# Kernel optimization log

Hardware: AMD Instinct MI355X
Metric: run time of the kernel (lower is better)

The kernel has to match this reference:

```python
import jax, jax.numpy as jnp
import numpy as np

NUM_HEADS = 8
SCALE = 1.0  # args.pos_mlp_scale


def setup_inputs() -> dict:
    key = jax.random.key(0)
    ks = jax.random.split(key, 6)
    B, N, dim = 2, 384, 256
    hid = dim // 2

    def xavier(k, fan_in, fan_out):
        lim = np.sqrt(6.0 / (fan_in + fan_out)).astype(np.float32)
        return jax.random.uniform(k, (fan_in, fan_out), jnp.float32, -lim, lim)

    return {
        "x": jax.random.normal(ks[0], (B, N, dim), jnp.float32),
        "pos": jax.random.normal(ks[1], (B, N, 3), jnp.float32),
        "mask": jnp.zeros((B, N), dtype=bool),  # True = padded position
        "qkv_w": xavier(ks[2], dim, 3 * dim),
        "qkv_b": jnp.zeros((3 * dim,), jnp.float32),
        "pm_w1": xavier(ks[3], 1, hid),
        "pm_b1": jnp.zeros((hid,), jnp.float32),
        "pm_w2": xavier(ks[4], hid, dim),
        "pm_b2": jnp.zeros((dim,), jnp.float32),
        "out_w": xavier(ks[5], dim, dim),
        "out_b": jnp.zeros((dim,), jnp.float32),
    }


def reference(x, pos, mask, qkv_w, qkv_b, pm_w1, pm_b1, pm_w2, pm_b2, out_w, out_b):
    B, N, dim = x.shape
    H = NUM_HEADS
    hd = dim // H

    qkv = x @ qkv_w + qkv_b                                  # [B,N,3*dim]
    x_q, x_k, x_v = jnp.split(qkv, 3, axis=-1)

    rel = pos[:, :, None, :] - pos[:, None, :, :]            # [B,N,N,3]
    # use_distance=True: safe L2 norm (zero subgradient on the diagonal)
    sq = jnp.sum(rel * rel, axis=-1, keepdims=True)          # [B,N,N,1]
    d = jnp.sqrt(jnp.where(sq > 0, sq, 1.0)) * (sq > 0)
    rel_pos = SCALE * (jax.nn.relu(d @ pm_w1 + pm_b1) @ pm_w2 + pm_b2)  # [B,N,N,dim]

    # attn_weight_type == 'normal': w[b,i,j] = k_i * q_j + rel_pos[b,i,j]
    w = x_k[:, :, None, :] * x_q[:, None, :, :] + rel_pos    # [B,N,N,dim]
    w = w.reshape(B, N, N, H, hd)

    pair_mask = (mask[:, :, None] & mask[:, None, :])[:, :, :, None, None]
    w = jnp.where(pair_mask, -jnp.inf, w)
    w = jax.nn.softmax(w, axis=2)                            # softmax over j

    # value_without_relpos=False: v[b,i,j] = x_v[b,j] + rel_pos[b,i,j]
    v = (x_v[:, None, :, :] + rel_pos).reshape(B, N, N, H, hd)
    out = jnp.sum(v * w, axis=2).reshape(B, N, dim)          # reduce over j
    return out @ out_w + out_b
```

## Files before the change

### kernel.cpp

```cpp
#include <hip/hip_runtime.h>
#include <hip/hip_bf16.h>

#define BB 2
#define NN 384
#define DIM 256
#define HID 128
#define ROWS (BB*NN)
#define LOG2E 1.4426950408889634f

typedef __attribute__((ext_vector_type(8))) short bf16x8;
typedef __attribute__((ext_vector_type(4))) float f32x4;

static __device__ __forceinline__ unsigned int f2bf(float f) {
    unsigned int u = __builtin_bit_cast(unsigned int, f);
    return (u + 0x7FFFu + ((u >> 16) & 1u)) >> 16;
}

__global__ __launch_bounds__(256) void qkv_gemm(const float* __restrict__ x,
        const float* __restrict__ w, const float* __restrict__ bias,
        float* __restrict__ q, float* __restrict__ k, float* __restrict__ v,
        const float* __restrict__ w2, unsigned short* __restrict__ w2t) {
    __shared__ float xs[6][DIM];
    const int r0 = blockIdx.x * 6;
    const int t = threadIdx.x;

    {
        int g = blockIdx.x * 256 + t;
        w2t[(g & 255) * HID + (g >> 8)] = (unsigned short)f2bf(w2[g]);
    }

    #pragma unroll
    for (int i = 0; i < 6; ++i) xs[i][t] = x[(r0 + i) * DIM + t];
    __syncthreads();
    float acc[6][3];
    #pragma unroll
    for (int r = 0; r < 6; ++r) { acc[r][0]=0.f; acc[r][1]=0.f; acc[r][2]=0.f; }
    for (int kk0 = 0; kk0 < DIM; kk0 += 4) {
        float4 xv[6];
        #pragma unroll
        for (int r = 0; r < 6; ++r) xv[r] = *(const float4*)&xs[r][kk0];
        #pragma unroll
        for (int kk = 0; kk < 4; ++kk) {
            float w0  = w[(kk0+kk)*768 + t];
            float w1v = w[(kk0+kk)*768 + t + 256];
            float w2v = w[(kk0+kk)*768 + t + 512];
            #pragma unroll
            for (int r = 0; r < 6; ++r) {
                float xr = kk==0?xv[r].x : kk==1?xv[r].y : kk==2?xv[r].z : xv[r].w;
                acc[r][0] += xr*w0; acc[r][1] += xr*w1v; acc[r][2] += xr*w2v;
            }
        }
    }
    const float bq = bias[t], bk = bias[t+256], bv = bias[t+512];
    #pragma unroll
    for (int r = 0; r < 6; ++r) {
        q[(r0+r)*DIM + t] = acc[r][0] + bq;
        k[(r0+r)*DIM + t] = acc[r][1] + bk;
        v[(r0+r)*DIM + t] = acc[r][2] + bv;
    }
}

__global__ __launch_bounds__(512, 4) void attn_main(
        const float* __restrict__ q,
        const float* __restrict__ k,
        const float* __restrict__ v,
        const float* __restrict__ pos,
        const unsigned char* __restrict__ mask,
        const float* __restrict__ w1,
        const float* __restrict__ b1,
        const unsigned short* __restrict__ w2t,
        const float* __restrict__ b2,
        float* __restrict__ out_pre)
{
    __shared__ char smem[65536];
    unsigned short (*w2l)[HID] = (unsigned short (*)[HID])smem;
    unsigned short (*hl)[HID]  = (unsigned short (*)[HID])smem;
    float* dl  = (float*)(smem + 8192);
    float* w1s = (float*)(smem + 8448);
    float* b1s = (float*)(smem + 8960);

    const int tid = threadIdx.x;
    const int row = blockIdx.x;
    const int b = row / NN;
    const int l = tid & 63;
    const int wv = tid >> 6;
    const int lc = l & 15, lr = l >> 4;
    const int c0 = wv * 32;

    #pragma unroll
    for (int it = 0; it < 8; ++it) {
        int f = tid + (it << 9);
        int c = f >> 4, u = f & 15;
        int up = u ^ ((c & 3) << 2);
        *(uint4*)&w2l[c][up * 8] = *(const uint4*)(w2t + c * HID + u * 8);
    }
    __syncthreads();

    bf16x8 Bc[2][4];
    #pragma unroll
    for (int ct = 0; ct < 2; ++ct) {
        int c = c0 + ct * 16 + lc;
        #pragma unroll
        for (int kk = 0; kk < 4; ++kk) {
            int up = (kk * 4 + lr) ^ ((c & 3) << 2);
            Bc[ct][kk] = *(const bf16x8*)&w2l[c][up * 8];
        }
    }
    __syncthreads();

    const float pix = pos[row*3+0], piy = pos[row*3+1], piz = pos[row*3+2];
    if (tid < HID) { w1s[tid] = w1[tid]; b1s[tid] = b1[tid]; }
    if (tid < 32) {
        int jg = b*NN + tid;
        float dx = pix - pos[jg*3+0], dy = piy - pos[jg*3+1], dz = piz - pos[jg*3+2];
        float sq = dx*dx + dy*dy + dz*dz;
        dl[tid] = sq > 0.f ? sqrtf(sq) : 0.f;
    }

    float kq2[2], b2v[2], b2c[2];
    #pragma unroll
    for (int ct = 0; ct < 2; ++ct) {
        int c = c0 + ct * 16 + lc;
        float kq = k[row * DIM + c];
        kq2[ct] = kq * LOG2E;
        b2v[ct] = b2[c];
        b2c[ct] = (b2v[ct] - 20.f) * LOG2E;
    }
    const bool mi = mask[row] != 0;

    float s[2] = {0.f, 0.f}, o[2] = {0.f, 0.f};

    const int jl_ = tid >> 4;
    const int u_  = tid & 15;
    const int up_ = u_ ^ ((jl_ & 7) << 1);

    for (int t = 0; t < 12; ++t) {
        const int jb = t * 32;
        __syncthreads();
        {
            float d = dl[(t & 1) * 32 + jl_];
            if (tid < 32 && jb + 32 < NN) {
                int jg = b*NN + jb + 32 + tid;
                float dx = pix - pos[jg*3+0], dy = piy - pos[jg*3+1], dz = piz - pos[jg*3+2];
                float sq = dx*dx + dy*dy + dz*dz;
                dl[((t+1) & 1) * 32 + tid] = sq > 0.f ? sqrtf(sq) : 0.f;
            }
            float4 wa = *(const float4*)&w1s[u_*8];
            float4 wb = *(const float4*)&w1s[u_*8+4];
            float4 ba = *(const float4*)&b1s[u_*8];
            float4 bb = *(const float4*)&b1s[u_*8+4];
            float h0 = fmaxf(fmaf(d, wa.x, ba.x), 0.f), h1 = fmaxf(fmaf(d, wa.y, ba.y), 0.f);
            float h2 = fmaxf(fmaf(d, wa.z, ba.z), 0.f), h3 = fmaxf(fmaf(d, wa.w, ba.w), 0.f);
            float h4 = fmaxf(fmaf(d, wb.x, bb.x), 0.f), h5 = fmaxf(fmaf(d, wb.y, bb.y), 0.f);
            float h6 = fmaxf(fmaf(d, wb.z, bb.z), 0.f), h7 = fmaxf(fmaf(d, wb.w, bb.w), 0.f);
            uint4 pkt;
            pkt.x = f2bf(h0) | (f2bf(h1) << 16);
            pkt.y = f2bf(h2) | (f2bf(h3) << 16);
            pkt.z = f2bf(h4) | (f2bf(h5) << 16);
            pkt.w = f2bf(h6) | (f2bf(h7) << 16);
            *(uint4*)&hl[jl_][up_ * 8] = pkt;
        }
        __syncthreads();

        #pragma unroll
        for (int jt = 0; jt < 2; ++jt) {
            bf16x8 Af[4];
            #pragma unroll
            for (int kk = 0; kk < 4; ++kk) {
                int jl = jt * 16 + lc;
                int up = (kk * 4 + lr) ^ ((jl & 7) << 1);
                Af[kk] = *(const bf16x8*)&hl[jl][up * 8];
            }
            const int jg0 = b * NN + jb + jt * 16 + (lr << 2);
            float qr[2][4], vr[2][4];
            f32x4 acc[2];
            #pragma unroll
            for (int ct = 0; ct < 2; ++ct) {
                const int c = c0 + ct * 16 + lc;
                const float* qp = q + jg0 * DIM + c;
                const float* vp = v + jg0 * DIM + c;
                #pragma unroll
                for (int r = 0; r < 4; ++r) { qr[ct][r] = qp[r * DIM]; vr[ct][r] = vp[r * DIM]; }
                acc[ct] = (f32x4){0.f, 0.f, 0.f, 0.f};
                #pragma unroll
                for (int kk = 0; kk < 4; ++kk)
                    acc[ct] = __builtin_amdgcn_mfma_f32_16x16x32_bf16(Af[kk], Bc[ct][kk], acc[ct], 0, 0, 0);
            }
            #pragma unroll
            for (int ct = 0; ct < 2; ++ct) {
                #pragma unroll
                for (int r = 0; r < 4; ++r) {
                    float rp   = acc[ct][r] + b2v[ct];
                    float t1   = fmaf(acc[ct][r], LOG2E, b2c[ct]);
                    float lgt2 = fmaf(kq2[ct], qr[ct][r], t1);
                    float p = exp2f(lgt2);
                    if (mi && mask[jg0 + r]) p = 0.f;
                    s[ct] += p;
                    o[ct] = fmaf(p, vr[ct][r] + rp, o[ct]);
                }
            }
        }
    }

    #pragma unroll
    for (int ct = 0; ct < 2; ++ct) {
        float sv = s[ct], ov = o[ct];
        sv += __shfl_xor(sv, 16, 64); ov += __shfl_xor(ov, 16, 64);
        sv += __shfl_xor(sv, 32, 64); ov += __shfl_xor(ov, 32, 64);
        if (l < 16) out_pre[row * DIM + c0 + ct * 16 + l] = ov / sv;
    }
}

__global__ __launch_bounds__(256) void out_gemm(const float* __restrict__ a,
        const float* __restrict__ w, const float* __restrict__ bias,
        float* __restrict__ out) {
    __shared__ float as[6][DIM];
    const int r0 = blockIdx.x * 6;
    const int t = threadIdx.x;
    #pragma unroll
    for (int i = 0; i < 6; ++i) as[i][t] = a[(r0 + i) * DIM + t];
    __syncthreads();
    float acc[6] = {0.f, 0.f, 0.f, 0.f, 0.f, 0.f};
    for (int kk0 = 0; kk0 < DIM; kk0 += 4) {
        float4 xv[6];
        #pragma unroll
        for (int r = 0; r < 6; ++r) xv[r] = *(const float4*)&as[r][kk0];
        #pragma unroll
        for (int kk = 0; kk < 4; ++kk) {
            float wv = w[(kk0+kk)*DIM + t];
            #pragma unroll
            for (int r = 0; r < 6; ++r) {
                float xr = kk==0?xv[r].x : kk==1?xv[r].y : kk==2?xv[r].z : xv[r].w;
                acc[r] += xr * wv;
            }
        }
    }
    #pragma unroll
    for (int r = 0; r < 6; ++r) out[(r0+r)*DIM + t] = acc[r] + bias[t];
}

extern "C" void kernel_launch(void* const* d_in, const int* in_sizes, int n_in,
                              void* d_out, int out_size, void* d_ws, size_t ws_size,
                              hipStream_t stream) {
    const float* x      = (const float*)d_in[0];
    const float* pos    = (const float*)d_in[1];
    const unsigned char* mask = (const unsigned char*)d_in[2];
    const float* qkv_w  = (const float*)d_in[3];
    const float* qkv_b  = (const float*)d_in[4];
    const float* pm_w1  = (const float*)d_in[5];
    const float* pm_b1  = (const float*)d_in[6];
    const float* pm_w2  = (const float*)d_in[7];
    const float* pm_b2  = (const float*)d_in[8];
    const float* out_w  = (const float*)d_in[9];
    const float* out_b  = (const float*)d_in[10];
    float* out = (float*)d_out;

    char* ws = (char*)d_ws;
    float* qb           = (float*)(ws);
    float* kb           = (float*)(ws +  786432);
    float* vb           = (float*)(ws + 1572864);
    float* out_pre      = (float*)(ws + 2359296);
    unsigned short* w2t = (unsigned short*)(ws + 3145728);

    hipLaunchKernelGGL(qkv_gemm, dim3(ROWS/6), dim3(256), 0, stream,
                       x, qkv_w, qkv_b, qb, kb, vb, pm_w2, w2t);
    hipLaunchKernelGGL(attn_main, dim3(ROWS), dim3(512), 0, stream,
                       qb, kb, vb, pos, mask, pm_w1, pm_b1, w2t, pm_b2, out_pre);
    hipLaunchKernelGGL(out_gemm, dim3(ROWS/6), dim3(256), 0, stream, out_pre, out_w, out_b, out);
}
```

Before: 85.64 us.

## Interleave q/v buffers, shrink shared memory, and double j-tile size in attention

Stores q and v interleaved as float2 so each attention lane issues one 8-byte load per row instead of two scalar loads. Cuts the shared buffer from 64KB to about 18KB by staging w2 in four 32-wide slices, which lets more blocks fit per CU. Processes 64 j-positions per tile (6 iterations instead of 12), halving the barriers, and folds the b2 bias into the MFMA accumulator initialisation. It also uses the hardware bf16 pack intrinsic and a refined swizzle. The cost is more synchronisation during w2 staging and higher per-iteration register use.

```diff
diff --git a/kernel.cpp b/kernel.cpp
--- a/kernel.cpp
+++ b/kernel.cpp
@@ -1,5 +1,6 @@
 #include <hip/hip_runtime.h>
 #include <hip/hip_bf16.h>
+#include <string.h>
 
 #define BB 2
 #define NN 384
@@ -15,10 +16,15 @@
     unsigned int u = __builtin_bit_cast(unsigned int, f);
     return (u + 0x7FFFu + ((u >> 16) & 1u)) >> 16;
 }
+static __device__ __forceinline__ unsigned int pack2bf(float lo, float hi) {
+    __hip_bfloat162 h = __float22bfloat162_rn(float2{lo, hi});
+    unsigned int w; __builtin_memcpy(&w, &h, 4);
+    return w;
+}
 
 __global__ __launch_bounds__(256) void qkv_gemm(const float* __restrict__ x,
         const float* __restrict__ w, const float* __restrict__ bias,
-        float* __restrict__ q, float* __restrict__ k, float* __restrict__ v,
+        float2* __restrict__ qv, float* __restrict__ k,
         const float* __restrict__ w2, unsigned short* __restrict__ w2t) {
     __shared__ float xs[6][DIM];
     const int r0 = blockIdx.x * 6;
@@ -54,16 +60,16 @@
     const float bq = bias[t], bk = bias[t+256], bv = bias[t+512];
     #pragma unroll
     for (int r = 0; r < 6; ++r) {
-        q[(r0+r)*DIM + t] = acc[r][0] + bq;
-        k[(r0+r)*DIM + t] = acc[r][1] + bk;
-        v[(r0+r)*DIM + t] = acc[r][2] + bv;
-    }
-}
+        qv[(r0+r)*DIM + t] = float2{acc[r][0] + bq, acc[r][2] + bv};
+        k[(r0+r)*DIM + t]  = acc[r][1] + bk;
+    }
+}
+
+#define SWZ(jl, u) ((u) ^ (((jl) & 7) << 1) ^ (((jl) >> 3) & 1))
 
 __global__ __launch_bounds__(512, 4) void attn_main(
-        const float* __restrict__ q,
+        const float2* __restrict__ qv,
         const float* __restrict__ k,
-        const float* __restrict__ v,
         const float* __restrict__ pos,
         const unsigned char* __restrict__ mask,
         const float* __restrict__ w1,
@@ -72,12 +78,12 @@
         const float* __restrict__ b2,
         float* __restrict__ out_pre)
 {
-    __shared__ char smem[65536];
-    unsigned short (*w2l)[HID] = (unsigned short (*)[HID])smem;
-    unsigned short (*hl)[HID]  = (unsigned short (*)[HID])smem;
-    float* dl  = (float*)(smem + 8192);
-    float* w1s = (float*)(smem + 8448);
-    float* b1s = (float*)(smem + 8960);
+    __shared__ char smem[17920];
+    unsigned short (*w2s)[32] = (unsigned short (*)[32])smem;
+    unsigned short (*hl)[HID] = (unsigned short (*)[HID])smem;
+    float* dl  = (float*)(smem + 16384);
+    float* w1s = (float*)(smem + 16896);
+    float* b1s = (float*)(smem + 17408);
 
     const int tid = threadIdx.x;
     const int row = blockIdx.x;
@@ -87,101 +93,99 @@
     const int lc = l & 15, lr = l >> 4;
     const int c0 = wv * 32;
 
-    #pragma unroll
-    for (int it = 0; it < 8; ++it) {
-        int f = tid + (it << 9);
-        int c = f >> 4, u = f & 15;
-        int up = u ^ ((c & 3) << 2);
-        *(uint4*)&w2l[c][up * 8] = *(const uint4*)(w2t + c * HID + u * 8);
-    }
-    __syncthreads();
-
     bf16x8 Bc[2][4];
     #pragma unroll
-    for (int ct = 0; ct < 2; ++ct) {
-        int c = c0 + ct * 16 + lc;
-        #pragma unroll
-        for (int kk = 0; kk < 4; ++kk) {
-            int up = (kk * 4 + lr) ^ ((c & 3) << 2);
-            Bc[ct][kk] = *(const bf16x8*)&w2l[c][up * 8];
-        }
-    }
-    __syncthreads();
+    for (int P = 0; P < 4; ++P) {
+        #pragma unroll
+        for (int it = 0; it < 2; ++it) {
+            int f = tid + (it << 9);
+            int c = f >> 2, u = f & 3;
+            int up = u ^ ((c >> 1) & 3);
+            *(uint4*)&w2s[c][up * 8] = *(const uint4*)(w2t + c * HID + P * 32 + u * 8);
+        }
+        __syncthreads();
+        #pragma unroll
+        for (int ct = 0; ct < 2; ++ct) {
+            int c = c0 + ct * 16 + lc;
+            int up = lr ^ ((c >> 1) & 3);
+            Bc[ct][P] = *(const bf16x8*)&w2s[c][up * 8];
+        }
+        __syncthreads();
+    }
 
     const float pix = pos[row*3+0], piy = pos[row*3+1], piz = pos[row*3+2];
     if (tid < HID) { w1s[tid] = w1[tid]; b1s[tid] = b1[tid]; }
-    if (tid < 32) {
+    if (tid < 64) {
         int jg = b*NN + tid;
         float dx = pix - pos[jg*3+0], dy = piy - pos[jg*3+1], dz = piz - pos[jg*3+2];
         float sq = dx*dx + dy*dy + dz*dz;
         dl[tid] = sq > 0.f ? sqrtf(sq) : 0.f;
     }
 
-    float kq2[2], b2v[2], b2c[2];
+    float kq2[2], b2v[2];
     #pragma unroll
     for (int ct = 0; ct < 2; ++ct) {
         int c = c0 + ct * 16 + lc;
-        float kq = k[row * DIM + c];
-        kq2[ct] = kq * LOG2E;
+        kq2[ct] = k[row * DIM + c] * LOG2E;
         b2v[ct] = b2[c];
-        b2c[ct] = (b2v[ct] - 20.f) * LOG2E;
-    }
+    }
+    const float C20 = -20.f * LOG2E;
     const bool mi = mask[row] != 0;
 
     float s[2] = {0.f, 0.f}, o[2] = {0.f, 0.f};
 
     const int jl_ = tid >> 4;
     const int u_  = tid & 15;
-    const int up_ = u_ ^ ((jl_ & 7) << 1);
-
-    for (int t = 0; t < 12; ++t) {
-        const int jb = t * 32;
+
+    for (int t = 0; t < 6; ++t) {
+        const int jb = t * 64;
         __syncthreads();
         {
-            float d = dl[(t & 1) * 32 + jl_];
-            if (tid < 32 && jb + 32 < NN) {
-                int jg = b*NN + jb + 32 + tid;
-                float dx = pix - pos[jg*3+0], dy = piy - pos[jg*3+1], dz = piz - pos[jg*3+2];
-                float sq = dx*dx + dy*dy + dz*dz;
-                dl[((t+1) & 1) * 32 + tid] = sq > 0.f ? sqrtf(sq) : 0.f;
-            }
             float4 wa = *(const float4*)&w1s[u_*8];
             float4 wb = *(const float4*)&w1s[u_*8+4];
             float4 ba = *(const float4*)&b1s[u_*8];
             float4 bb = *(const float4*)&b1s[u_*8+4];
-            float h0 = fmaxf(fmaf(d, wa.x, ba.x), 0.f), h1 = fmaxf(fmaf(d, wa.y, ba.y), 0.f);
-            float h2 = fmaxf(fmaf(d, wa.z, ba.z), 0.f), h3 = fmaxf(fmaf(d, wa.w, ba.w), 0.f);
-            float h4 = fmaxf(fmaf(d, wb.x, bb.x), 0.f), h5 = fmaxf(fmaf(d, wb.y, bb.y), 0.f);
-            float h6 = fmaxf(fmaf(d, wb.z, bb.z), 0.f), h7 = fmaxf(fmaf(d, wb.w, bb.w), 0.f);
-            uint4 pkt;
-            pkt.x = f2bf(h0) | (f2bf(h1) << 16);
-            pkt.y = f2bf(h2) | (f2bf(h3) << 16);
-            pkt.z = f2bf(h4) | (f2bf(h5) << 16);
-            pkt.w = f2bf(h6) | (f2bf(h7) << 16);
-            *(uint4*)&hl[jl_][up_ * 8] = pkt;
-        }
-        __syncthreads();
-
-        #pragma unroll
-        for (int jt = 0; jt < 2; ++jt) {
+            #pragma unroll
+            for (int it = 0; it < 2; ++it) {
+                int jl = jl_ + it * 32;
+                float d = dl[(t & 1) * 64 + jl];
+                float h0 = fmaxf(fmaf(d, wa.x, ba.x), 0.f), h1 = fmaxf(fmaf(d, wa.y, ba.y), 0.f);
+                float h2 = fmaxf(fmaf(d, wa.z, ba.z), 0.f), h3 = fmaxf(fmaf(d, wa.w, ba.w), 0.f);
+                float h4 = fmaxf(fmaf(d, wb.x, bb.x), 0.f), h5 = fmaxf(fmaf(d, wb.y, bb.y), 0.f);
+                float h6 = fmaxf(fmaf(d, wb.z, bb.z), 0.f), h7 = fmaxf(fmaf(d, wb.w, bb.w), 0.f);
+                uint4 pkt;
+                pkt.x = pack2bf(h0, h1);
+                pkt.y = pack2bf(h2, h3);
+                pkt.z = pack2bf(h4, h5);
+                pkt.w = pack2bf(h6, h7);
+                *(uint4*)&hl[jl][SWZ(jl, u_) * 8] = pkt;
+            }
+            if (tid < 64 && jb + 64 < NN) {
+                int jg = b*NN + jb + 64 + tid;
+                float dx = pix - pos[jg*3+0], dy = piy - pos[jg*3+1], dz = piz - pos[jg*3+2];
+                float sq = dx*dx + dy*dy + dz*dz;
+                dl[((t+1) & 1) * 64 + tid] = sq > 0.f ? sqrtf(sq) : 0.f;
+            }
+        }
+        __syncthreads();
+
+        #pragma unroll
+        for (int jt = 0; jt < 4; ++jt) {
+            const int jl0 = jt * 16 + lc;
             bf16x8 Af[4];
             #pragma unroll
-            for (int kk = 0; kk < 4; ++kk) {
-                int jl = jt * 16 + lc;
-                int up = (kk * 4 + lr) ^ ((jl & 7) << 1);
-                Af[kk] = *(const bf16x8*)&hl[jl][up * 8];
-            }
+            for (int kk = 0; kk < 4; ++kk)
+                Af[kk] = *(const bf16x8*)&hl[jl0][SWZ(jl0, kk * 4 + lr) * 8];
+
             const int jg0 = b * NN + jb + jt * 16 + (lr << 2);
-            float qr[2][4], vr[2][4];
+            float2 q2[2][4];
             f32x4 acc[2];
             #pragma unroll
             for (int ct = 0; ct < 2; ++ct) {
-                const int c = c0 + ct * 16 + lc;
-                const float* qp = q + jg0 * DIM + c;
-                const float* vp = v + jg0 * DIM + c;
+                const float2* basep = qv + (jg0) * DIM + c0 + ct * 16 + lc;
                 #pragma unroll
-                for (int r = 0; r < 4; ++r) { qr[ct][r] = qp[r * DIM]; vr[ct][r] = vp[r * DIM]; }
-                acc[ct] = (f32x4){0.f, 0.f, 0.f, 0.f};
+                for (int r = 0; r < 4; ++r) q2[ct][r] = basep[r * DIM];
+                acc[ct] = (f32x4){b2v[ct], b2v[ct], b2v[ct], b2v[ct]};
                 #pragma unroll
                 for (int kk = 0; kk < 4; ++kk)
                     acc[ct] = __builtin_amdgcn_mfma_f32_16x16x32_bf16(Af[kk], Bc[ct][kk], acc[ct], 0, 0, 0);
@@ -190,13 +194,13 @@
             for (int ct = 0; ct < 2; ++ct) {
                 #pragma unroll
                 for (int r = 0; r < 4; ++r) {
-                    float rp   = acc[ct][r] + b2v[ct];
-                    float t1   = fmaf(acc[ct][r], LOG2E, b2c[ct]);
-                    float lgt2 = fmaf(kq2[ct], qr[ct][r], t1);
+                    float rp   = acc[ct][r];
+                    float t1   = fmaf(rp, LOG2E, C20);
+                    float lgt2 = fmaf(kq2[ct], q2[ct][r].x, t1);
                     float p = exp2f(lgt2);
                     if (mi && mask[jg0 + r]) p = 0.f;
                     s[ct] += p;
-                    o[ct] = fmaf(p, vr[ct][r] + rp, o[ct]);
+                    o[ct] = fmaf(p, q2[ct][r].y + rp, o[ct]);
                 }
             }
         }
@@ -256,15 +260,14 @@
     float* out = (float*)d_out;
 
     char* ws = (char*)d_ws;
-    float* qb           = (float*)(ws);
-    float* kb           = (float*)(ws +  786432);
-    float* vb           = (float*)(ws + 1572864);
+    float2* qvb         = (float2*)(ws);
+    float* kb           = (float*)(ws + 1572864);
     float* out_pre      = (float*)(ws + 2359296);
     unsigned short* w2t = (unsigned short*)(ws + 3145728);
 
     hipLaunchKernelGGL(qkv_gemm, dim3(ROWS/6), dim3(256), 0, stream,
-                       x, qkv_w, qkv_b, qb, kb, vb, pm_w2, w2t);
+                       x, qkv_w, qkv_b, qvb, kb, pm_w2, w2t);
     hipLaunchKernelGGL(attn_main, dim3(ROWS), dim3(512), 0, stream,
-                       qb, kb, vb, pos, mask, pm_w1, pm_b1, w2t, pm_b2, out_pre);
+                       qvb, kb, pos, mask, pm_w1, pm_b1, w2t, pm_b2, out_pre);
     hipLaunchKernelGGL(out_gemm, dim3(ROWS/6), dim3(256), 0, stream, out_pre, out_w, out_b, out);
 }
```

After: 210.2 us. 145% more time.

## Process two query rows per attention block to reuse q/v loads

Applied to the files above, without the earlier changes.

Each attention block now handles two rows i, so every q and v value loaded from global memory feeds two softmax accumulations. Tiles grow to 64 keys and the LDS footprint is cut so more blocks fit per CU. W2 is staged through LDS in four chunks and the hidden-tile swizzle gains an extra bit. The qkv and output GEMMs go from six rows to three rows per block, doubling the grid. The trade-off is more registers per thread in attention and half as many attention blocks to spread across CUs.

```diff
diff --git a/kernel.cpp b/kernel.cpp
--- a/kernel.cpp
+++ b/kernel.cpp
@@ -16,36 +16,38 @@
     return (u + 0x7FFFu + ((u >> 16) & 1u)) >> 16;
 }
 
+#define SWZ(jl, u) ((u) ^ (((jl) & 7) << 1) ^ (((jl) >> 3) & 1))
+
 __global__ __launch_bounds__(256) void qkv_gemm(const float* __restrict__ x,
         const float* __restrict__ w, const float* __restrict__ bias,
         float* __restrict__ q, float* __restrict__ k, float* __restrict__ v,
         const float* __restrict__ w2, unsigned short* __restrict__ w2t) {
-    __shared__ float xs[6][DIM];
-    const int r0 = blockIdx.x * 6;
+    __shared__ float xs[3][DIM];
+    const int r0 = blockIdx.x * 3;
     const int t = threadIdx.x;
 
-    {
-        int g = blockIdx.x * 256 + t;
+    if (t < 128) {
+        int g = blockIdx.x * 128 + t;
         w2t[(g & 255) * HID + (g >> 8)] = (unsigned short)f2bf(w2[g]);
     }
 
     #pragma unroll
-    for (int i = 0; i < 6; ++i) xs[i][t] = x[(r0 + i) * DIM + t];
+    for (int i = 0; i < 3; ++i) xs[i][t] = x[(r0 + i) * DIM + t];
     __syncthreads();
-    float acc[6][3];
-    #pragma unroll
-    for (int r = 0; r < 6; ++r) { acc[r][0]=0.f; acc[r][1]=0.f; acc[r][2]=0.f; }
+    float acc[3][3];
+    #pragma unroll
+    for (int r = 0; r < 3; ++r) { acc[r][0]=0.f; acc[r][1]=0.f; acc[r][2]=0.f; }
     for (int kk0 = 0; kk0 < DIM; kk0 += 4) {
-        float4 xv[6];
-        #pragma unroll
-        for (int r = 0; r < 6; ++r) xv[r] = *(const float4*)&xs[r][kk0];
+        float4 xv[3];
+        #pragma unroll
+        for (int r = 0; r < 3; ++r) xv[r] = *(const float4*)&xs[r][kk0];
         #pragma unroll
         for (int kk = 0; kk < 4; ++kk) {
             float w0  = w[(kk0+kk)*768 + t];
             float w1v = w[(kk0+kk)*768 + t + 256];
             float w2v = w[(kk0+kk)*768 + t + 512];
             #pragma unroll
-            for (int r = 0; r < 6; ++r) {
+            for (int r = 0; r < 3; ++r) {
                 float xr = kk==0?xv[r].x : kk==1?xv[r].y : kk==2?xv[r].z : xv[r].w;
                 acc[r][0] += xr*w0; acc[r][1] += xr*w1v; acc[r][2] += xr*w2v;
             }
@@ -53,14 +55,15 @@
     }
     const float bq = bias[t], bk = bias[t+256], bv = bias[t+512];
     #pragma unroll
-    for (int r = 0; r < 6; ++r) {
+    for (int r = 0; r < 3; ++r) {
         q[(r0+r)*DIM + t] = acc[r][0] + bq;
         k[(r0+r)*DIM + t] = acc[r][1] + bk;
         v[(r0+r)*DIM + t] = acc[r][2] + bv;
     }
 }
 
-__global__ __launch_bounds__(512, 4) void attn_main(
+__global__ __attribute__((amdgpu_waves_per_eu(4, 4))) __launch_bounds__(512)
+void attn_main(
         const float* __restrict__ q,
         const float* __restrict__ k,
         const float* __restrict__ v,
@@ -72,171 +75,189 @@
         const float* __restrict__ b2,
         float* __restrict__ out_pre)
 {
-    __shared__ char smem[65536];
-    unsigned short (*w2l)[HID] = (unsigned short (*)[HID])smem;
-    unsigned short (*hl)[HID]  = (unsigned short (*)[HID])smem;
-    float* dl  = (float*)(smem + 8192);
-    float* w1s = (float*)(smem + 8448);
-    float* b1s = (float*)(smem + 8960);
+    __shared__ char smem[34816];
+    unsigned short (*w2s)[32] = (unsigned short (*)[32])smem;
+    unsigned short (*hl)[64][HID] = (unsigned short (*)[64][HID])smem;
+    float* dl  = (float*)(smem + 32768);
+    float* w1s = (float*)(smem + 33792);
+    float* b1s = (float*)(smem + 34304);
 
     const int tid = threadIdx.x;
-    const int row = blockIdx.x;
-    const int b = row / NN;
+    const int row0 = blockIdx.x * 2;
+    const int b = row0 / NN;
     const int l = tid & 63;
     const int wv = tid >> 6;
     const int lc = l & 15, lr = l >> 4;
     const int c0 = wv * 32;
 
-    #pragma unroll
-    for (int it = 0; it < 8; ++it) {
-        int f = tid + (it << 9);
-        int c = f >> 4, u = f & 15;
-        int up = u ^ ((c & 3) << 2);
-        *(uint4*)&w2l[c][up * 8] = *(const uint4*)(w2t + c * HID + u * 8);
-    }
-    __syncthreads();
-
     bf16x8 Bc[2][4];
+    #pragma unroll
+    for (int P = 0; P < 4; ++P) {
+        #pragma unroll
+        for (int it = 0; it < 2; ++it) {
+            int f = tid + (it << 9);
+            int c = f >> 2, u = f & 3;
+            int up = u ^ ((c >> 1) & 3);
+            *(uint4*)&w2s[c][up * 8] = *(const uint4*)(w2t + c * HID + P * 32 + u * 8);
+        }
+        __syncthreads();
+        #pragma unroll
+        for (int ct = 0; ct < 2; ++ct) {
+            int c = c0 + ct * 16 + lc;
+            int up = lr ^ ((c >> 1) & 3);
+            Bc[ct][P] = *(const bf16x8*)&w2s[c][up * 8];
+        }
+        __syncthreads();
+    }
+
+    const float pix0 = pos[row0*3+0], piy0 = pos[row0*3+1], piz0 = pos[row0*3+2];
+    const float pix1 = pos[row0*3+3], piy1 = pos[row0*3+4], piz1 = pos[row0*3+5];
+    if (tid < HID) { w1s[tid] = w1[tid]; b1s[tid] = b1[tid]; }
+    if (tid < 128) {
+        int i = tid >> 6, jj = tid & 63;
+        float px = i ? pix1 : pix0, py = i ? piy1 : piy0, pz = i ? piz1 : piz0;
+        int jg = b*NN + jj;
+        float dx = px - pos[jg*3+0], dy = py - pos[jg*3+1], dz = pz - pos[jg*3+2];
+        float sq = dx*dx + dy*dy + dz*dz;
+        dl[i*64 + jj] = sq > 0.f ? sqrtf(sq) : 0.f;
+    }
+
+    float kq2[2][2], b2v[2], b2c[2];
     #pragma unroll
     for (int ct = 0; ct < 2; ++ct) {
         int c = c0 + ct * 16 + lc;
-        #pragma unroll
-        for (int kk = 0; kk < 4; ++kk) {
-            int up = (kk * 4 + lr) ^ ((c & 3) << 2);
-            Bc[ct][kk] = *(const bf16x8*)&w2l[c][up * 8];
-        }
-    }
-    __syncthreads();
-
-    const float pix = pos[row*3+0], piy = pos[row*3+1], piz = pos[row*3+2];
-    if (tid < HID) { w1s[tid] = w1[tid]; b1s[tid] = b1[tid]; }
-    if (tid < 32) {
-        int jg = b*NN + tid;
-        float dx = pix - pos[jg*3+0], dy = piy - pos[jg*3+1], dz = piz - pos[jg*3+2];
-        float sq = dx*dx + dy*dy + dz*dz;
-        dl[tid] = sq > 0.f ? sqrtf(sq) : 0.f;
-    }
-
-    float kq2[2], b2v[2], b2c[2];
-    #pragma unroll
-    for (int ct = 0; ct < 2; ++ct) {
-        int c = c0 + ct * 16 + lc;
-        float kq = k[row * DIM + c];
-        kq2[ct] = kq * LOG2E;
+        kq2[0][ct] = k[row0 * DIM + c] * LOG2E;
+        kq2[1][ct] = k[(row0 + 1) * DIM + c] * LOG2E;
         b2v[ct] = b2[c];
         b2c[ct] = (b2v[ct] - 20.f) * LOG2E;
     }
-    const bool mi = mask[row] != 0;
-
-    float s[2] = {0.f, 0.f}, o[2] = {0.f, 0.f};
-
-    const int jl_ = tid >> 4;
-    const int u_  = tid & 15;
-    const int up_ = u_ ^ ((jl_ & 7) << 1);
-
-    for (int t = 0; t < 12; ++t) {
-        const int jb = t * 32;
+    const bool mi0 = mask[row0] != 0, mi1 = mask[row0 + 1] != 0;
+
+    float s[2][2] = {{0.f,0.f},{0.f,0.f}}, o[2][2] = {{0.f,0.f},{0.f,0.f}};
+
+    const int u_ = tid & 15;
+    const int jlb = tid >> 4;
+
+    for (int t = 0; t < 6; ++t) {
+        const int jb = t * 64;
         __syncthreads();
         {
-            float d = dl[(t & 1) * 32 + jl_];
-            if (tid < 32 && jb + 32 < NN) {
-                int jg = b*NN + jb + 32 + tid;
-                float dx = pix - pos[jg*3+0], dy = piy - pos[jg*3+1], dz = piz - pos[jg*3+2];
-                float sq = dx*dx + dy*dy + dz*dz;
-                dl[((t+1) & 1) * 32 + tid] = sq > 0.f ? sqrtf(sq) : 0.f;
-            }
             float4 wa = *(const float4*)&w1s[u_*8];
             float4 wb = *(const float4*)&w1s[u_*8+4];
             float4 ba = *(const float4*)&b1s[u_*8];
             float4 bb = *(const float4*)&b1s[u_*8+4];
-            float h0 = fmaxf(fmaf(d, wa.x, ba.x), 0.f), h1 = fmaxf(fmaf(d, wa.y, ba.y), 0.f);
-            float h2 = fmaxf(fmaf(d, wa.z, ba.z), 0.f), h3 = fmaxf(fmaf(d, wa.w, ba.w), 0.f);
-            float h4 = fmaxf(fmaf(d, wb.x, bb.x), 0.f), h5 = fmaxf(fmaf(d, wb.y, bb.y), 0.f);
-            float h6 = fmaxf(fmaf(d, wb.z, bb.z), 0.f), h7 = fmaxf(fmaf(d, wb.w, bb.w), 0.f);
-            uint4 pkt;
-            pkt.x = f2bf(h0) | (f2bf(h1) << 16);
-            pkt.y = f2bf(h2) | (f2bf(h3) << 16);
-            pkt.z = f2bf(h4) | (f2bf(h5) << 16);
-            pkt.w = f2bf(h6) | (f2bf(h7) << 16);
-            *(uint4*)&hl[jl_][up_ * 8] = pkt;
-        }
-        __syncthreads();
-
-        #pragma unroll
-        for (int jt = 0; jt < 2; ++jt) {
-            bf16x8 Af[4];
-            #pragma unroll
-            for (int kk = 0; kk < 4; ++kk) {
-                int jl = jt * 16 + lc;
-                int up = (kk * 4 + lr) ^ ((jl & 7) << 1);
-                Af[kk] = *(const bf16x8*)&hl[jl][up * 8];
-            }
+            #pragma unroll
+            for (int it = 0; it < 4; ++it) {
+                const int i = it >> 1;
+                const int jl = jlb + (it & 1) * 32;
+                float d = dl[(t & 1) * 128 + i * 64 + jl];
+                float h0 = fmaxf(fmaf(d, wa.x, ba.x), 0.f), h1 = fmaxf(fmaf(d, wa.y, ba.y), 0.f);
+                float h2 = fmaxf(fmaf(d, wa.z, ba.z), 0.f), h3 = fmaxf(fmaf(d, wa.w, ba.w), 0.f);
+                float h4 = fmaxf(fmaf(d, wb.x, bb.x), 0.f), h5 = fmaxf(fmaf(d, wb.y, bb.y), 0.f);
+                float h6 = fmaxf(fmaf(d, wb.z, bb.z), 0.f), h7 = fmaxf(fmaf(d, wb.w, bb.w), 0.f);
+                uint4 pkt;
+                pkt.x = f2bf(h0) | (f2bf(h1) << 16);
+                pkt.y = f2bf(h2) | (f2bf(h3) << 16);
+                pkt.z = f2bf(h4) | (f2bf(h5) << 16);
+                pkt.w = f2bf(h6) | (f2bf(h7) << 16);
+                *(uint4*)&hl[i][jl][SWZ(jl, u_) * 8] = pkt;
+            }
+            if (t < 5 && tid < 128) {
+                int i = tid >> 6, jj = tid & 63;
+                float px = i ? pix1 : pix0, py = i ? piy1 : piy0, pz = i ? piz1 : piz0;
+                int jg = b*NN + jb + 64 + jj;
+                float dx = px - pos[jg*3+0], dy = py - pos[jg*3+1], dz = pz - pos[jg*3+2];
+                float sq = dx*dx + dy*dy + dz*dz;
+                dl[((t + 1) & 1) * 128 + i * 64 + jj] = sq > 0.f ? sqrtf(sq) : 0.f;
+            }
+        }
+        __syncthreads();
+
+        #pragma unroll
+        for (int jt = 0; jt < 4; ++jt) {
+            const int jl0 = jt * 16 + lc;
             const int jg0 = b * NN + jb + jt * 16 + (lr << 2);
             float qr[2][4], vr[2][4];
-            f32x4 acc[2];
             #pragma unroll
             for (int ct = 0; ct < 2; ++ct) {
-                const int c = c0 + ct * 16 + lc;
-                const float* qp = q + jg0 * DIM + c;
-                const float* vp = v + jg0 * DIM + c;
+                const float* qp = q + jg0 * DIM + c0 + ct * 16 + lc;
+                const float* vp = v + jg0 * DIM + c0 + ct * 16 + lc;
                 #pragma unroll
                 for (int r = 0; r < 4; ++r) { qr[ct][r] = qp[r * DIM]; vr[ct][r] = vp[r * DIM]; }
-                acc[ct] = (f32x4){0.f, 0.f, 0.f, 0.f};
+            }
+            f32x4 acc[2][2];
+            #pragma unroll
+            for (int i = 0; i < 2; ++i) {
+                bf16x8 Af[4];
                 #pragma unroll
                 for (int kk = 0; kk < 4; ++kk)
-                    acc[ct] = __builtin_amdgcn_mfma_f32_16x16x32_bf16(Af[kk], Bc[ct][kk], acc[ct], 0, 0, 0);
-            }
-            #pragma unroll
-            for (int ct = 0; ct < 2; ++ct) {
-                #pragma unroll
-                for (int r = 0; r < 4; ++r) {
-                    float rp   = acc[ct][r] + b2v[ct];
-                    float t1   = fmaf(acc[ct][r], LOG2E, b2c[ct]);
-                    float lgt2 = fmaf(kq2[ct], qr[ct][r], t1);
-                    float p = exp2f(lgt2);
-                    if (mi && mask[jg0 + r]) p = 0.f;
-                    s[ct] += p;
-                    o[ct] = fmaf(p, vr[ct][r] + rp, o[ct]);
+                    Af[kk] = *(const bf16x8*)&hl[i][jl0][SWZ(jl0, kk * 4 + lr) * 8];
+                #pragma unroll
+                for (int ct = 0; ct < 2; ++ct) {
+                    acc[i][ct] = (f32x4){0.f, 0.f, 0.f, 0.f};
+                    #pragma unroll
+                    for (int kk = 0; kk < 4; ++kk)
+                        acc[i][ct] = __builtin_amdgcn_mfma_f32_16x16x32_bf16(Af[kk], Bc[ct][kk], acc[i][ct], 0, 0, 0);
                 }
             }
-        }
-    }
-
-    #pragma unroll
-    for (int ct = 0; ct < 2; ++ct) {
-        float sv = s[ct], ov = o[ct];
-        sv += __shfl_xor(sv, 16, 64); ov += __shfl_xor(ov, 16, 64);
-        sv += __shfl_xor(sv, 32, 64); ov += __shfl_xor(ov, 32, 64);
-        if (l < 16) out_pre[row * DIM + c0 + ct * 16 + l] = ov / sv;
+            #pragma unroll
+            for (int i = 0; i < 2; ++i) {
+                const bool mi = i ? mi1 : mi0;
+                #pragma unroll
+                for (int ct = 0; ct < 2; ++ct) {
+                    #pragma unroll
+                    for (int r = 0; r < 4; ++r) {
+                        float a  = acc[i][ct][r];
+                        float rp = a + b2v[ct];
+                        float lgt2 = fmaf(kq2[i][ct], qr[ct][r], fmaf(a, LOG2E, b2c[ct]));
+                        float p = exp2f(lgt2);
+                        if (mi && mask[jg0 + r]) p = 0.f;
+                        s[i][ct] += p;
+                        o[i][ct] = fmaf(p, vr[ct][r] + rp, o[i][ct]);
+                    }
+                }
+            }
+        }
+    }
+
+    #pragma unroll
+    for (int i = 0; i < 2; ++i) {
+        #pragma unroll
+        for (int ct = 0; ct < 2; ++ct) {
+            float sv = s[i][ct], ov = o[i][ct];
+            sv += __shfl_xor(sv, 16, 64); ov += __shfl_xor(ov, 16, 64);
+            sv += __shfl_xor(sv, 32, 64); ov += __shfl_xor(ov, 32, 64);
+            if (l < 16) out_pre[(row0 + i) * DIM + c0 + ct * 16 + l] = ov / sv;
+        }
     }
 }
 
 __global__ __launch_bounds__(256) void out_gemm(const float* __restrict__ a,
         const float* __restrict__ w, const float* __restrict__ bias,
         float* __restrict__ out) {
-    __shared__ float as[6][DIM];
-    const int r0 = blockIdx.x * 6;
+    __shared__ float as[3][DIM];
+    const int r0 = blockIdx.x * 3;
     const int t = threadIdx.x;
     #pragma unroll
-    for (int i = 0; i < 6; ++i) as[i][t] = a[(r0 + i) * DIM + t];
+    for (int i = 0; i < 3; ++i) as[i][t] = a[(r0 + i) * DIM + t];
     __syncthreads();
-    float acc[6] = {0.f, 0.f, 0.f, 0.f, 0.f, 0.f};
+    float acc[3] = {0.f, 0.f, 0.f};
     for (int kk0 = 0; kk0 < DIM; kk0 += 4) {
-        float4 xv[6];
-        #pragma unroll
-        for (int r = 0; r < 6; ++r) xv[r] = *(const float4*)&as[r][kk0];
+        float4 xv[3];
+        #pragma unroll
+        for (int r = 0; r < 3; ++r) xv[r] = *(const float4*)&as[r][kk0];
         #pragma unroll
         for (int kk = 0; kk < 4; ++kk) {
             float wv = w[(kk0+kk)*DIM + t];
             #pragma unroll
-            for (int r = 0; r < 6; ++r) {
+            for (int r = 0; r < 3; ++r) {
                 float xr = kk==0?xv[r].x : kk==1?xv[r].y : kk==2?xv[r].z : xv[r].w;
                 acc[r] += xr * wv;
             }
         }
     }
     #pragma unroll
-    for (int r = 0; r < 6; ++r) out[(r0+r)*DIM + t] = acc[r] + bias[t];
+    for (int r = 0; r < 3; ++r) out[(r0+r)*DIM + t] = acc[r] + bias[t];
 }
 
 extern "C" void kernel_launch(void* const* d_in, const int* in_sizes, int n_in,
@@ -262,9 +283,9 @@
     float* out_pre      = (float*)(ws + 2359296);
     unsigned short* w2t = (unsigned short*)(ws + 3145728);
 
-    hipLaunchKernelGGL(qkv_gemm, dim3(ROWS/6), dim3(256), 0, stream,
+    hipLaunchKernelGGL(qkv_gemm, dim3(ROWS/3), dim3(256), 0, stream,
                        x, qkv_w, qkv_b, qb, kb, vb, pm_w2, w2t);
-    hipLaunchKernelGGL(attn_main, dim3(ROWS), dim3(512), 0, stream,
+    hipLaunchKernelGGL(attn_main, dim3(ROWS/2), dim3(512), 0, stream,
                        qb, kb, vb, pos, mask, pm_w1, pm_b1, w2t, pm_b2, out_pre);
-    hipLaunchKernelGGL(out_gemm, dim3(ROWS/6), dim3(256), 0, stream, out_pre, out_w, out_b, out);
-}
+    hipLaunchKernelGGL(out_gemm, dim3(ROWS/3), dim3(256), 0, stream, out_pre, out_w, out_b, out);
+}
```

Result: slower. 272.4 us (+218.1%).

## Store q and v transposed for vectorized loads and shrink attention LDS footprint

Applied to the files above, without the earlier changes.

The QKV GEMM now writes q and v in a column-major [DIM][ROWS] layout and is retiled to 16 rows by 64 columns per block, which gives 192 blocks. This lets the attention kernel fetch four consecutive j values per lane with a single float4 load instead of four strided scalar loads. The attention kernel also stages w2 through a 16KB LDS buffer in four chunks instead of a 64KB buffer, which lowers LDS use per block and could raise occupancy. The chunked staging adds extra barriers at block start, and the w2t conversion now needs a bounds guard because the new grid size no longer matches it.

```diff
diff --git a/kernel.cpp b/kernel.cpp
--- a/kernel.cpp
+++ b/kernel.cpp
@@ -16,54 +16,65 @@
     return (u + 0x7FFFu + ((u >> 16) & 1u)) >> 16;
 }
 
-__global__ __launch_bounds__(256) void qkv_gemm(const float* __restrict__ x,
+__global__ __launch_bounds__(256, 2) void qkv_gemm(const float* __restrict__ x,
         const float* __restrict__ w, const float* __restrict__ bias,
-        float* __restrict__ q, float* __restrict__ k, float* __restrict__ v,
+        float* __restrict__ qt, float* __restrict__ k, float* __restrict__ vt,
         const float* __restrict__ w2, unsigned short* __restrict__ w2t) {
-    __shared__ float xs[6][DIM];
-    const int r0 = blockIdx.x * 6;
+    __shared__ float xs[16][DIM];
+    const int r0    = (blockIdx.x >> 2) * 16;
+    const int cbase = (blockIdx.x & 3) * 64;
     const int t = threadIdx.x;
+    const int ci = t & 63;
+    const int rq = t >> 6;
 
     {
         int g = blockIdx.x * 256 + t;
-        w2t[(g & 255) * HID + (g >> 8)] = (unsigned short)f2bf(w2[g]);
-    }
-
-    #pragma unroll
-    for (int i = 0; i < 6; ++i) xs[i][t] = x[(r0 + i) * DIM + t];
+        if (g < 32768) w2t[(g & 255) * HID + (g >> 8)] = (unsigned short)f2bf(w2[g]);
+    }
+
+    #pragma unroll
+    for (int i = 0; i < 16; ++i) xs[i][t] = x[(r0 + i) * DIM + t];
     __syncthreads();
-    float acc[6][3];
-    #pragma unroll
-    for (int r = 0; r < 6; ++r) { acc[r][0]=0.f; acc[r][1]=0.f; acc[r][2]=0.f; }
+
+    const int c = cbase + ci;
+    float acc[4][3];
+    #pragma unroll
+    for (int r = 0; r < 4; ++r) { acc[r][0]=0.f; acc[r][1]=0.f; acc[r][2]=0.f; }
     for (int kk0 = 0; kk0 < DIM; kk0 += 4) {
-        float4 xv[6];
-        #pragma unroll
-        for (int r = 0; r < 6; ++r) xv[r] = *(const float4*)&xs[r][kk0];
+        float wc[4][3];
         #pragma unroll
         for (int kk = 0; kk < 4; ++kk) {
-            float w0  = w[(kk0+kk)*768 + t];
-            float w1v = w[(kk0+kk)*768 + t + 256];
-            float w2v = w[(kk0+kk)*768 + t + 512];
-            #pragma unroll
-            for (int r = 0; r < 6; ++r) {
-                float xr = kk==0?xv[r].x : kk==1?xv[r].y : kk==2?xv[r].z : xv[r].w;
-                acc[r][0] += xr*w0; acc[r][1] += xr*w1v; acc[r][2] += xr*w2v;
-            }
-        }
-    }
-    const float bq = bias[t], bk = bias[t+256], bv = bias[t+512];
-    #pragma unroll
-    for (int r = 0; r < 6; ++r) {
-        q[(r0+r)*DIM + t] = acc[r][0] + bq;
-        k[(r0+r)*DIM + t] = acc[r][1] + bk;
-        v[(r0+r)*DIM + t] = acc[r][2] + bv;
-    }
+            wc[kk][0] = w[(kk0+kk)*768 + c];
+            wc[kk][1] = w[(kk0+kk)*768 + c + 256];
+            wc[kk][2] = w[(kk0+kk)*768 + c + 512];
+        }
+        float4 xv[4];
+        #pragma unroll
+        for (int rr = 0; rr < 4; ++rr) xv[rr] = *(const float4*)&xs[rq*4+rr][kk0];
+        #pragma unroll
+        for (int kk = 0; kk < 4; ++kk) {
+            #pragma unroll
+            for (int rr = 0; rr < 4; ++rr) {
+                float xr = kk==0?xv[rr].x : kk==1?xv[rr].y : kk==2?xv[rr].z : xv[rr].w;
+                acc[rr][0] += xr*wc[kk][0];
+                acc[rr][1] += xr*wc[kk][1];
+                acc[rr][2] += xr*wc[kk][2];
+            }
+        }
+    }
+    const float bq = bias[c], bk = bias[c+256], bv = bias[c+512];
+    float4 qo = {acc[0][0]+bq, acc[1][0]+bq, acc[2][0]+bq, acc[3][0]+bq};
+    float4 vo = {acc[0][2]+bv, acc[1][2]+bv, acc[2][2]+bv, acc[3][2]+bv};
+    *(float4*)&qt[c*ROWS + r0 + rq*4] = qo;
+    *(float4*)&vt[c*ROWS + r0 + rq*4] = vo;
+    #pragma unroll
+    for (int rr = 0; rr < 4; ++rr) k[(r0 + rq*4 + rr)*DIM + c] = acc[rr][1] + bk;
 }
 
 __global__ __launch_bounds__(512, 4) void attn_main(
-        const float* __restrict__ q,
+        const float* __restrict__ qt,
         const float* __restrict__ k,
-        const float* __restrict__ v,
+        const float* __restrict__ vt,
         const float* __restrict__ pos,
         const unsigned char* __restrict__ mask,
         const float* __restrict__ w1,
@@ -72,12 +83,12 @@
         const float* __restrict__ b2,
         float* __restrict__ out_pre)
 {
-    __shared__ char smem[65536];
-    unsigned short (*w2l)[HID] = (unsigned short (*)[HID])smem;
-    unsigned short (*hl)[HID]  = (unsigned short (*)[HID])smem;
-    float* dl  = (float*)(smem + 8192);
-    float* w1s = (float*)(smem + 8448);
-    float* b1s = (float*)(smem + 8960);
+    __shared__ char smem[17664];
+    unsigned short (*w2s)[32] = (unsigned short (*)[32])smem;
+    unsigned short (*hl)[HID] = (unsigned short (*)[HID])smem;
+    float* dl  = (float*)(smem + 16384);
+    float* w1s = (float*)(smem + 16640);
+    float* b1s = (float*)(smem + 17152);
 
     const int tid = threadIdx.x;
     const int row = blockIdx.x;
@@ -87,26 +98,25 @@
     const int lc = l & 15, lr = l >> 4;
     const int c0 = wv * 32;
 
-    #pragma unroll
-    for (int it = 0; it < 8; ++it) {
-        int f = tid + (it << 9);
-        int c = f >> 4, u = f & 15;
-        int up = u ^ ((c & 3) << 2);
-        *(uint4*)&w2l[c][up * 8] = *(const uint4*)(w2t + c * HID + u * 8);
-    }
-    __syncthreads();
-
     bf16x8 Bc[2][4];
     #pragma unroll
-    for (int ct = 0; ct < 2; ++ct) {
-        int c = c0 + ct * 16 + lc;
-        #pragma unroll
-        for (int kk = 0; kk < 4; ++kk) {
-            int up = (kk * 4 + lr) ^ ((c & 3) << 2);
-            Bc[ct][kk] = *(const bf16x8*)&w2l[c][up * 8];
-        }
-    }
-    __syncthreads();
+    for (int P = 0; P < 4; ++P) {
+        #pragma unroll
+        for (int it = 0; it < 2; ++it) {
+            int f = tid + (it << 9);
+            int c = f >> 2, u = f & 3;
+            int up = u ^ ((c >> 1) & 3);
+            *(uint4*)&w2s[c][up * 8] = *(const uint4*)(w2t + c * HID + P * 32 + u * 8);
+        }
+        __syncthreads();
+        #pragma unroll
+        for (int ct = 0; ct < 2; ++ct) {
+            int c = c0 + ct * 16 + lc;
+            int up = lr ^ ((c >> 1) & 3);
+            Bc[ct][P] = *(const bf16x8*)&w2s[c][up * 8];
+        }
+        __syncthreads();
+    }
 
     const float pix = pos[row*3+0], piy = pos[row*3+1], piz = pos[row*3+2];
     if (tid < HID) { w1s[tid] = w1[tid]; b1s[tid] = b1[tid]; }
@@ -118,13 +128,14 @@
     }
 
     float kq2[2], b2v[2], b2c[2];
+    int qoff[2];
     #pragma unroll
     for (int ct = 0; ct < 2; ++ct) {
         int c = c0 + ct * 16 + lc;
-        float kq = k[row * DIM + c];
-        kq2[ct] = kq * LOG2E;
+        kq2[ct] = k[row * DIM + c] * LOG2E;
         b2v[ct] = b2[c];
         b2c[ct] = (b2v[ct] - 20.f) * LOG2E;
+        qoff[ct] = c * ROWS + b * NN + (lr << 2);
     }
     const bool mi = mask[row] != 0;
 
@@ -164,23 +175,21 @@
 
         #pragma unroll
         for (int jt = 0; jt < 2; ++jt) {
+            const int jl0 = jt * 16 + lc;
             bf16x8 Af[4];
             #pragma unroll
             for (int kk = 0; kk < 4; ++kk) {
-                int jl = jt * 16 + lc;
-                int up = (kk * 4 + lr) ^ ((jl & 7) << 1);
-                Af[kk] = *(const bf16x8*)&hl[jl][up * 8];
+                int up = (kk * 4 + lr) ^ ((jl0 & 7) << 1);
+                Af[kk] = *(const bf16x8*)&hl[jl0][up * 8];
             }
             const int jg0 = b * NN + jb + jt * 16 + (lr << 2);
-            float qr[2][4], vr[2][4];
+            float4 q4[2], v4[2];
             f32x4 acc[2];
             #pragma unroll
             for (int ct = 0; ct < 2; ++ct) {
-                const int c = c0 + ct * 16 + lc;
-                const float* qp = q + jg0 * DIM + c;
-                const float* vp = v + jg0 * DIM + c;
-                #pragma unroll
-                for (int r = 0; r < 4; ++r) { qr[ct][r] = qp[r * DIM]; vr[ct][r] = vp[r * DIM]; }
+                const int off = qoff[ct] + jb + jt * 16;
+                q4[ct] = *(const float4*)(qt + off);
+                v4[ct] = *(const float4*)(vt + off);
                 acc[ct] = (f32x4){0.f, 0.f, 0.f, 0.f};
                 #pragma unroll
                 for (int kk = 0; kk < 4; ++kk)
@@ -190,13 +199,15 @@
             for (int ct = 0; ct < 2; ++ct) {
                 #pragma unroll
                 for (int r = 0; r < 4; ++r) {
-                    float rp   = acc[ct][r] + b2v[ct];
-                    float t1   = fmaf(acc[ct][r], LOG2E, b2c[ct]);
-                    float lgt2 = fmaf(kq2[ct], qr[ct][r], t1);
+                    float a  = acc[ct][r];
+                    float rp = a + b2v[ct];
+                    float qv = r==0?q4[ct].x : r==1?q4[ct].y : r==2?q4[ct].z : q4[ct].w;
+                    float vv = r==0?v4[ct].x : r==1?v4[ct].y : r==2?v4[ct].z : v4[ct].w;
+                    float lgt2 = fmaf(kq2[ct], qv, fmaf(a, LOG2E, b2c[ct]));
                     float p = exp2f(lgt2);
                     if (mi && mask[jg0 + r]) p = 0.f;
                     s[ct] += p;
-                    o[ct] = fmaf(p, vr[ct][r] + rp, o[ct]);
+                    o[ct] = fmaf(p, vv + rp, o[ct]);
                 }
             }
         }
@@ -256,15 +267,15 @@
     float* out = (float*)d_out;
 
     char* ws = (char*)d_ws;
-    float* qb           = (float*)(ws);
+    float* qtb          = (float*)(ws);
     float* kb           = (float*)(ws +  786432);
-    float* vb           = (float*)(ws + 1572864);
+    float* vtb          = (float*)(ws + 1572864);
     float* out_pre      = (float*)(ws + 2359296);
     unsigned short* w2t = (unsigned short*)(ws + 3145728);
 
-    hipLaunchKernelGGL(qkv_gemm, dim3(ROWS/6), dim3(256), 0, stream,
-                       x, qkv_w, qkv_b, qb, kb, vb, pm_w2, w2t);
+    hipLaunchKernelGGL(qkv_gemm, dim3(192), dim3(256), 0, stream,
+                       x, qkv_w, qkv_b, qtb, kb, vtb, pm_w2, w2t);
     hipLaunchKernelGGL(attn_main, dim3(ROWS), dim3(512), 0, stream,
-                       qb, kb, vb, pos, mask, pm_w1, pm_b1, w2t, pm_b2, out_pre);
+                       qtb, kb, vtb, pos, mask, pm_w1, pm_b1, w2t, pm_b2, out_pre);
     hipLaunchKernelGGL(out_gemm, dim3(ROWS/6), dim3(256), 0, stream, out_pre, out_w, out_b, out);
 }
```

Result: slower. 112.1 us (+30.8%).
